# Performance work log

Measured on AMD Instinct MI355X. Metric: run time of the kernel, lower is better.

The kernel has to match this reference:

```python
import jax, jax.numpy as jnp
import numpy as np

B, S, D = 2, 1024, 1024
H, HD = 16, 64          # n_heads, head_dim (H*HD == D)
E, FF = 8, 2816         # num_experts, moe hidden_dim
TOP_K = 2               # hard-coded torch.topk(scores, 2)
EPS = 1e-5


def rmsnorm(x, w):
    return x * jax.lax.rsqrt(jnp.mean(x * x, axis=-1, keepdims=True) + EPS) * w


def apply_rope(x, cos, sin):
    # x: [B,S,H,HD]; cos/sin: [S,HD//2] -> interleaved rotary (llama style)
    xr, xi = x[..., 0::2], x[..., 1::2]
    c = cos[None, :, None, :]
    s = sin[None, :, None, :]
    out_r = xr * c - xi * s
    out_i = xr * s + xi * c
    return jnp.stack([out_r, out_i], axis=-1).reshape(x.shape)


def setup_inputs() -> dict:
    key = jax.random.key(0)
    ks = jax.random.split(key, 10)
    sc = 0.02
    pos = jnp.arange(S, dtype=jnp.float32)
    inv = 1.0 / (10000.0 ** (jnp.arange(0, HD, 2, dtype=jnp.float32) / HD))
    ang = pos[:, None] * inv[None, :]                       # [S, HD//2]
    return {
        "x": jax.random.normal(ks[0], (B, S, D), jnp.float32),
        "freqs_cos": jnp.cos(ang),
        "freqs_sin": jnp.sin(ang),
        "attn_norm_w": jnp.ones((D,), jnp.float32),
        "wq": jax.random.normal(ks[1], (D, D), jnp.float32) * sc,
        "wk": jax.random.normal(ks[2], (D, D), jnp.float32) * sc,
        "wv": jax.random.normal(ks[3], (D, D), jnp.float32) * sc,
        "wo": jax.random.normal(ks[4], (D, D), jnp.float32) * sc,
        "ffn_norm_w": jnp.ones((D,), jnp.float32),
        "gate_w": jax.random.normal(ks[5], (E, D), jnp.float32) * sc,
        "w1": jax.random.normal(ks[6], (E, FF, D), jnp.float32) * sc,
        "w2": jax.random.normal(ks[7], (E, FF, D), jnp.float32) * sc,
        "w3": jax.random.normal(ks[8], (E, FF, D), jnp.float32) * sc,
    }


def reference(x, freqs_cos, freqs_sin, attn_norm_w, wq, wk, wv, wo,
              ffn_norm_w, gate_w, w1, w2, w3):
    b, s, d = x.shape

    # ---- pre-norm attention + residual ----
    xn = rmsnorm(x, attn_norm_w)
    q = (xn @ wq.T).reshape(b, s, H, HD)
    k = (xn @ wk.T).reshape(b, s, H, HD)
    v = (xn @ wv.T).reshape(b, s, H, HD)
    q = apply_rope(q, freqs_cos, freqs_sin)
    k = apply_rope(k, freqs_cos, freqs_sin)
    scores = jnp.einsum("bqhd,bkhd->bhqk", q, k) / jnp.sqrt(jnp.float32(HD))
    causal = jnp.tril(jnp.ones((s, s), bool))
    scores = jnp.where(causal[None, None], scores, jnp.finfo(scores.dtype).min)
    attn = jax.nn.softmax(scores, axis=-1)
    o = jnp.einsum("bhqk,bkhd->bqhd", attn, v).reshape(b, s, d) @ wo.T
    h = x + o

    # ---- top-2 MoE FFN (math identical to gather-per-token einsums) ----
    t = rmsnorm(h, ffn_norm_w).reshape(-1, d)               # [T, D]
    T = t.shape[0]
    gate = t @ gate_w.T                                     # [T, E]
    expert_weights, expert_idx = jax.lax.top_k(gate, TOP_K)
    expert_weights = jax.nn.softmax(expert_weights, axis=-1)  # [T, 2]

    x1 = jax.nn.silu(jnp.einsum("td,efd->tef", t, w1))      # [T, E, FF]
    x3 = jnp.einsum("td,efd->tef", t, w3)                   # [T, E, FF]
    ta = jnp.arange(T)[:, None]
    g = x1[ta, expert_idx] * x3[ta, expert_idx]             # [T, 2, FF]
    gw = g * expert_weights[..., None]                      # fold routing weights
    h_full = jnp.zeros((T, E, FF), t.dtype).at[ta, expert_idx].add(gw)
    moe = jnp.einsum("tef,efd->td", h_full, w2)             # [T, D]

    return h + moe.reshape(b, s, d)
```

## Files before the change

kernel.cpp:

```cpp
#include <hip/hip_runtime.h>

#define DI __device__ __forceinline__

typedef __attribute__((ext_vector_type(8))) short short8;
typedef __attribute__((ext_vector_type(4))) float f32x4;

#define DM   1024
#define TT   2048
#define SEQ  1024
#define NHD  16
#define HDD  64
#define NE   8
#define FF   2816

DI ushort f2bf(float f){
  union { float f; unsigned u; } c; c.f = f;
  unsigned u = c.u;
  u += 0x7fffu + ((u >> 16) & 1u);
  return (ushort)(u >> 16);
}
DI float bf2f(ushort b){
  union { unsigned u; float f; } c; c.u = ((unsigned)b) << 16;
  return c.f;
}
DI unsigned pk2(float a, float b){ return (unsigned)f2bf(a) | ((unsigned)f2bf(b) << 16); }
DI uint2 mku2(unsigned a, unsigned b){ uint2 r; r.x = a; r.y = b; return r; }

DI f32x4 MFMA(short8 a, short8 b, f32x4 c){
  return __builtin_amdgcn_mfma_f32_16x16x32_bf16(a, b, c, 0, 0, 0);
}

DI void gload16(const void* g, void* l){
  __builtin_amdgcn_global_load_lds(
      (const __attribute__((address_space(1))) unsigned*)g,
      (__attribute__((address_space(3))) unsigned*)l, 16, 0, 0);
}

#define LDSWZB(row, p) (((row) * 128) + ((((p) ^ ((row) & 7))) * 16))
#define WZ32(row, p)   (((row) * 256) + ((((p) ^ ((row) & 7))) * 16))

__global__ __launch_bounds__(256) void k_rmsnorm(const float* __restrict__ x,
                                                 const float* __restrict__ w,
                                                 ushort* __restrict__ xh,
                                                 ushort* __restrict__ xl)
{
  int row = blockIdx.x, tid = threadIdx.x;
  float4 v = ((const float4*)(x + (size_t)row * DM))[tid];
  float ss = v.x*v.x + v.y*v.y + v.z*v.z + v.w*v.w;
#pragma unroll
  for (int m = 32; m >= 1; m >>= 1) ss += __shfl_xor(ss, m);
  __shared__ float sh[4];
  if ((tid & 63) == 0) sh[tid >> 6] = ss;
  __syncthreads();
  ss = sh[0] + sh[1] + sh[2] + sh[3];
  float rstd = 1.0f / sqrtf(ss * (1.0f / DM) + 1e-5f);
  float4 wv = ((const float4*)w)[tid];
  float o0 = v.x * rstd * wv.x, o1 = v.y * rstd * wv.y;
  float o2 = v.z * rstd * wv.z, o3 = v.w * rstd * wv.w;
  ushort h0 = f2bf(o0), h1 = f2bf(o1), h2 = f2bf(o2), h3 = f2bf(o3);
  ((uint2*)(xh + (size_t)row * DM))[tid] =
      mku2((unsigned)h0 | ((unsigned)h1 << 16), (unsigned)h2 | ((unsigned)h3 << 16));
  ((uint2*)(xl + (size_t)row * DM))[tid] =
      mku2(pk2(o0 - bf2f(h0), o1 - bf2f(h1)), pk2(o2 - bf2f(h2), o3 - bf2f(h3)));
}

__global__ __launch_bounds__(256) void k_wsplit(
    const float* __restrict__ wq, const float* __restrict__ wk,
    const float* __restrict__ wv, const float* __restrict__ wo,
    ushort* __restrict__ qh, ushort* __restrict__ ql,
    ushort* __restrict__ kh, ushort* __restrict__ kl,
    ushort* __restrict__ vh, ushort* __restrict__ vl,
    ushort* __restrict__ oh, ushort* __restrict__ ol)
{
  int y = blockIdx.y;
  const float* W = y == 0 ? wq : (y == 1 ? wk : (y == 2 ? wv : wo));
  ushort* H = y == 0 ? qh : (y == 1 ? kh : (y == 2 ? vh : oh));
  ushort* L = y == 0 ? ql : (y == 1 ? kl : (y == 2 ? vl : ol));
  int i = blockIdx.x * 256 + threadIdx.x;
  float4 v = ((const float4*)W)[i];
  ushort h0 = f2bf(v.x), h1 = f2bf(v.y), h2 = f2bf(v.z), h3 = f2bf(v.w);
  ((uint2*)H)[i] = mku2((unsigned)h0 | ((unsigned)h1 << 16),
                        (unsigned)h2 | ((unsigned)h3 << 16));
  ((uint2*)L)[i] = mku2(pk2(v.x - bf2f(h0), v.y - bf2f(h1)),
                        pk2(v.z - bf2f(h2), v.w - bf2f(h3)));
}

__global__ __launch_bounds__(256, 2) void k_gemm_qkv(
    const ushort* __restrict__ xh, const ushort* __restrict__ xl,
    const ushort* __restrict__ wqh, const ushort* __restrict__ wql,
    const ushort* __restrict__ wkh, const ushort* __restrict__ wkl,
    const ushort* __restrict__ wvh, const ushort* __restrict__ wvl,
    float* __restrict__ qf, float* __restrict__ kf,
    ushort* __restrict__ vh, ushort* __restrict__ vl)
{
  __shared__ __align__(16) char lds[65536];
  char* Ah = lds;          char* Al = lds + 16384;
  char* Bh = lds + 32768;  char* Bl = lds + 49152;
  int bn = blockIdx.x, bm = blockIdx.y;
  int which = bn >> 3, bnn = bn & 7;
  const ushort* WH = which == 0 ? wqh : (which == 1 ? wkh : wvh);
  const ushort* WL = which == 0 ? wql : (which == 1 ? wkl : wvl);
  int tid = threadIdx.x, lane = tid & 63, w = tid >> 6, wr = w >> 1, wc = w & 1;
  int r0 = lane >> 3, pp = lane & 7;
  size_t asrc[4], bsrc[4]; int cdst[4];
#pragma unroll
  for (int i = 0; i < 4; i++) {
    int c = w * 4 + i;
    int row = c * 8 + r0;
    asrc[i] = (size_t)(bm * 128 + row) * DM + (pp ^ r0) * 8;
    bsrc[i] = (size_t)(bnn * 128 + row) * DM + (pp ^ r0) * 8;
    cdst[i] = c * 1024;
  }
  f32x4 acc[4][4] = {};
  for (int kb = 0; kb < DM; kb += 64) {
    __syncthreads();
#pragma unroll
    for (int i = 0; i < 4; i++) {
      gload16(xh + asrc[i] + kb, Ah + cdst[i]);
      gload16(xl + asrc[i] + kb, Al + cdst[i]);
      gload16(WH + bsrc[i] + kb, Bh + cdst[i]);
      gload16(WL + bsrc[i] + kb, Bl + cdst[i]);
    }
    __syncthreads();
#pragma unroll
    for (int kk = 0; kk < 2; kk++) {
      int j = kk * 4 + (lane >> 4);
      short8 ar[4], al[4];
#pragma unroll
      for (int mi = 0; mi < 4; mi++) {
        int row = wr * 64 + mi * 16 + (lane & 15);
        ar[mi] = *(const short8*)(Ah + LDSWZB(row, j));
        al[mi] = *(const short8*)(Al + LDSWZB(row, j));
      }
#pragma unroll
      for (int ni = 0; ni < 4; ni++) {
        int n = wc * 64 + ni * 16 + (lane & 15);
        short8 b_h = *(const short8*)(Bh + LDSWZB(n, j));
        short8 b_l = *(const short8*)(Bl + LDSWZB(n, j));
#pragma unroll
        for (int mi = 0; mi < 4; mi++) {
          acc[mi][ni] = MFMA(ar[mi], b_h, acc[mi][ni]);
          acc[mi][ni] = MFMA(al[mi], b_h, acc[mi][ni]);
          acc[mi][ni] = MFMA(ar[mi], b_l, acc[mi][ni]);
        }
      }
    }
  }
#pragma unroll
  for (int mi = 0; mi < 4; mi++)
#pragma unroll
    for (int ni = 0; ni < 4; ni++)
#pragma unroll
      for (int r = 0; r < 4; r++) {
        int rg = bm*128 + wr*64 + mi*16 + (lane >> 4)*4 + r;
        int cg = bnn*128 + wc*64 + ni*16 + (lane & 15);
        float v = acc[mi][ni][r];
        if (which == 0)      qf[(size_t)rg * DM + cg] = v;
        else if (which == 1) kf[(size_t)rg * DM + cg] = v;
        else {
          int b = rg >> 10, s = rg & 1023, hh = cg >> 6, hd = cg & 63;
          size_t o = ((size_t)((b*NHD + hh)*HDD + hd)) * SEQ + s;
          ushort hv = f2bf(v);
          vh[o] = hv; vl[o] = f2bf(v - bf2f(hv));
        }
      }
}

__global__ __launch_bounds__(256) void k_rope(
    const float* __restrict__ qf, const float* __restrict__ kf,
    const float* __restrict__ fc, const float* __restrict__ fs,
    ushort* __restrict__ qh, ushort* __restrict__ ql,
    ushort* __restrict__ kh, ushort* __restrict__ kl)
{
  int t = blockIdx.x, tid = threadIdx.x;
  int b = t >> 10, s = t & 1023;
#pragma unroll
  for (int i = 0; i < 2; i++) {
    int p = tid + i*256;
    int hh = p >> 5, pi = p & 31;
    float c = fc[s*32 + pi], sn = fs[s*32 + pi];
    size_t o = ((size_t)(b*NHD + hh) * SEQ + s) * HDD + pi*2;
    {
      float2 v = *(const float2*)(qf + (size_t)t * DM + hh*HDD + pi*2);
      float r0 = v.x*c - v.y*sn, r1 = v.x*sn + v.y*c;
      ushort a0 = f2bf(r0), a1 = f2bf(r1);
      *(unsigned*)(qh + o) = (unsigned)a0 | ((unsigned)a1 << 16);
      *(unsigned*)(ql + o) = pk2(r0 - bf2f(a0), r1 - bf2f(a1));
    }
    {
      float2 v = *(const float2*)(kf + (size_t)t * DM + hh*HDD + pi*2);
      float r0 = v.x*c - v.y*sn, r1 = v.x*sn + v.y*c;
      ushort a0 = f2bf(r0), a1 = f2bf(r1);
      *(unsigned*)(kh + o) = (unsigned)a0 | ((unsigned)a1 << 16);
      *(unsigned*)(kl + o) = pk2(r0 - bf2f(a0), r1 - bf2f(a1));
    }
  }
}

__global__ __launch_bounds__(256) void k_attn(
    const ushort* __restrict__ qh_, const ushort* __restrict__ ql_,
    const ushort* __restrict__ kh_, const ushort* __restrict__ kl_,
    const ushort* __restrict__ vh_, const ushort* __restrict__ vl_,
    ushort* __restrict__ oh_, ushort* __restrict__ ol_)
{
  __shared__ __align__(16) ushort Kh[64*64], Kl[64*64], Vh[64*64], Vl[64*64];
  __shared__ __align__(16) ushort Ph[4*16*64], Pl[4*16*64];
  int qt = blockIdx.x, bh = blockIdx.y;
  int tid = threadIdx.x, lane = tid & 63, w = tid >> 6;
  short8 qfh[2], qfl[2];
  int qrow = qt*64 + w*16 + (lane & 15);
#pragma unroll
  for (int ks = 0; ks < 2; ks++) {
    size_t g = ((size_t)bh * SEQ + qrow) * HDD + ks*32 + (lane >> 4)*8;
    qfh[ks] = *(const short8*)(qh_ + g);
    qfl[ks] = *(const short8*)(ql_ + g);
  }
  f32x4 oacc[4] = {};
  float mrun[4], lrun[4];
#pragma unroll
  for (int r = 0; r < 4; r++) { mrun[r] = -1e30f; lrun[r] = 0.0f; }

  for (int kt = 0; kt <= qt; kt++) {
    __syncthreads();
#pragma unroll
    for (int i = 0; i < 2; i++) {
      int c = tid + i*256, row = c >> 3, sl = c & 7;
      int d = row*64 + ((sl + row) & 7) * 8;
      size_t gk = ((size_t)bh * SEQ + kt*64 + row) * HDD + sl*8;
      *(uint4*)&Kh[d] = *(const uint4*)(kh_ + gk);
      *(uint4*)&Kl[d] = *(const uint4*)(kl_ + gk);
      size_t gv = ((size_t)bh * HDD + row) * SEQ + kt*64 + sl*8;
      *(uint4*)&Vh[d] = *(const uint4*)(vh_ + gv);
      *(uint4*)&Vl[d] = *(const uint4*)(vl_ + gv);
    }
    __syncthreads();
    f32x4 sa[4] = {};
#pragma unroll
    for (int j = 0; j < 4; j++) {
#pragma unroll
      for (int ks = 0; ks < 2; ks++) {
        int kr = j*16 + (lane & 15);
        int d = kr*64 + (((ks*4 + (lane >> 4)) + kr) & 7) * 8;
        short8 b_h = *(const short8*)&Kh[d];
        short8 b_l = *(const short8*)&Kl[d];
        sa[j] = MFMA(qfh[ks], b_h, sa[j]);
        sa[j] = MFMA(qfl[ks], b_h, sa[j]);
        sa[j] = MFMA(qfh[ks], b_l, sa[j]);
      }
    }
    float sv[4][4];
#pragma unroll
    for (int j = 0; j < 4; j++)
#pragma unroll
      for (int r = 0; r < 4; r++) {
        float xx = sa[j][r] * 0.125f;
        if (kt == qt) {
          int kv = j*16 + (lane & 15), qi = w*16 + (lane >> 4)*4 + r;
          if (kv > qi) xx = -1e30f;
        }
        sv[j][r] = xx;
      }
#pragma unroll
    for (int r = 0; r < 4; r++) {
      float mx = fmaxf(fmaxf(sv[0][r], sv[1][r]), fmaxf(sv[2][r], sv[3][r]));
#pragma unroll
      for (int m = 8; m >= 1; m >>= 1) mx = fmaxf(mx, __shfl_xor(mx, m));
      float mn = fmaxf(mrun[r], mx);
      float alp = __expf(mrun[r] - mn);
      mrun[r] = mn;
      float rs = 0.0f;
#pragma unroll
      for (int j = 0; j < 4; j++) { float pv = __expf(sv[j][r] - mn); sv[j][r] = pv; rs += pv; }
#pragma unroll
      for (int m = 8; m >= 1; m >>= 1) rs += __shfl_xor(rs, m);
      lrun[r] = lrun[r] * alp + rs;
#pragma unroll
      for (int hf = 0; hf < 4; hf++) oacc[hf][r] *= alp;
    }
#pragma unroll
    for (int j = 0; j < 4; j++)
#pragma unroll
      for (int r = 0; r < 4; r++) {
        int row = (lane >> 4)*4 + r, col = j*16 + (lane & 15);
        int d = w*1024 + row*64 + (((col >> 3) ^ (row & 7)) * 8) + (col & 7);
        ushort hv = f2bf(sv[j][r]);
        Ph[d] = hv; Pl[d] = f2bf(sv[j][r] - bf2f(hv));
      }
#pragma unroll
    for (int hf = 0; hf < 4; hf++) {
#pragma unroll
      for (int ks = 0; ks < 2; ks++) {
        int prow = lane & 15;
        int pg = ((ks*4 + (lane >> 4)) ^ (prow & 7)) * 8;
        short8 pfh = *(const short8*)&Ph[w*1024 + prow*64 + pg];
        short8 pfl = *(const short8*)&Pl[w*1024 + prow*64 + pg];
        int vrow = hf*16 + (lane & 15);
        int vd = vrow*64 + (((ks*4 + (lane >> 4)) + vrow) & 7) * 8;
        short8 vfh = *(const short8*)&Vh[vd];
        short8 vfl = *(const short8*)&Vl[vd];
        oacc[hf] = MFMA(pfh, vfh, oacc[hf]);
        oacc[hf] = MFMA(pfl, vfh, oacc[hf]);
        oacc[hf] = MFMA(pfh, vfl, oacc[hf]);
      }
    }
  }
  int b = bh >> 4, h = bh & 15;
#pragma unroll
  for (int r = 0; r < 4; r++) {
    float li = 1.0f / lrun[r];
    int srow = qt*64 + w*16 + (lane >> 4)*4 + r;
#pragma unroll
    for (int hf = 0; hf < 4; hf++) {
      float v = oacc[hf][r] * li;
      size_t o = ((size_t)(b*SEQ + srow)) * DM + h*HDD + hf*16 + (lane & 15);
      ushort hv = f2bf(v);
      oh_[o] = hv; ol_[o] = f2bf(v - bf2f(hv));
    }
  }
}

__global__ __launch_bounds__(256, 2) void k_gemm_wo(
    const ushort* __restrict__ oh, const ushort* __restrict__ ol,
    const ushort* __restrict__ woh, const ushort* __restrict__ wol,
    const float* __restrict__ x, float* __restrict__ hb)
{
  __shared__ __align__(16) char lds[49152];
  char* Ah = lds;          char* Al = lds + 8192;
  char* Bh = lds + 16384;  char* Bl = lds + 32768;
  int bnn = blockIdx.x, bm = blockIdx.y;
  int tid = threadIdx.x, lane = tid & 63, w = tid >> 6;
  int r0 = lane >> 3, pp = lane & 7;
  size_t asrc[2]; int adst[2];
#pragma unroll
  for (int i = 0; i < 2; i++) {
    int c = w * 2 + i;
    int row = c * 8 + r0;
    asrc[i] = (size_t)(bm * 64 + row) * DM + (pp ^ r0) * 8;
    adst[i] = c * 1024;
  }
  size_t bsrc[4]; int bdst[4];
#pragma unroll
  for (int i = 0; i < 4; i++) {
    int c = w * 4 + i;
    int row = c * 8 + r0;
    bsrc[i] = (size_t)(bnn * 128 + row) * DM + (pp ^ r0) * 8;
    bdst[i] = c * 1024;
  }
  f32x4 acc[4][2] = {};
  for (int kb = 0; kb < DM; kb += 64) {
    __syncthreads();
#pragma unroll
    for (int i = 0; i < 2; i++) {
      gload16(oh + asrc[i] + kb, Ah + adst[i]);
      gload16(ol + asrc[i] + kb, Al + adst[i]);
    }
#pragma unroll
    for (int i = 0; i < 4; i++) {
      gload16(woh + bsrc[i] + kb, Bh + bdst[i]);
      gload16(wol + bsrc[i] + kb, Bl + bdst[i]);
    }
    __syncthreads();
#pragma unroll
    for (int kk = 0; kk < 2; kk++) {
      int j = kk * 4 + (lane >> 4);
      short8 ar[4], al[4];
#pragma unroll
      for (int mi = 0; mi < 4; mi++) {
        int row = mi * 16 + (lane & 15);
        ar[mi] = *(const short8*)(Ah + LDSWZB(row, j));
        al[mi] = *(const short8*)(Al + LDSWZB(row, j));
      }
#pragma unroll
      for (int ni = 0; ni < 2; ni++) {
        int n = w * 32 + ni * 16 + (lane & 15);
        short8 b_h = *(const short8*)(Bh + LDSWZB(n, j));
        short8 b_l = *(const short8*)(Bl + LDSWZB(n, j));
#pragma unroll
        for (int mi = 0; mi < 4; mi++) {
          acc[mi][ni] = MFMA(ar[mi], b_h, acc[mi][ni]);
          acc[mi][ni] = MFMA(al[mi], b_h, acc[mi][ni]);
          acc[mi][ni] = MFMA(ar[mi], b_l, acc[mi][ni]);
        }
      }
    }
  }
#pragma unroll
  for (int mi = 0; mi < 4; mi++)
#pragma unroll
    for (int ni = 0; ni < 2; ni++)
#pragma unroll
      for (int r = 0; r < 4; r++) {
        int rg = bm*64 + mi*16 + (lane >> 4)*4 + r;
        int cg = bnn*128 + w*32 + ni*16 + (lane & 15);
        hb[(size_t)rg * DM + cg] = x[(size_t)rg * DM + cg] + acc[mi][ni][r];
      }
}

__global__ __launch_bounds__(256) void k_gate(
    const float* __restrict__ hb, const float* __restrict__ fw, const float* __restrict__ gwt,
    ushort* __restrict__ tb, int* __restrict__ idx, float* __restrict__ ew, int* __restrict__ cnt)
{
  int t = blockIdx.x, tid = threadIdx.x;
  float4 v = ((const float4*)(hb + (size_t)t * DM))[tid];
  float ss = v.x*v.x + v.y*v.y + v.z*v.z + v.w*v.w;
#pragma unroll
  for (int m = 32; m >= 1; m >>= 1) ss += __shfl_xor(ss, m);
  __shared__ float sh[4];
  if ((tid & 63) == 0) sh[tid >> 6] = ss;
  __syncthreads();
  ss = sh[0] + sh[1] + sh[2] + sh[3];
  float rstd = 1.0f / sqrtf(ss * (1.0f / DM) + 1e-5f);
  float4 wv = ((const float4*)fw)[tid];
  float tv0 = v.x*rstd*wv.x, tv1 = v.y*rstd*wv.y, tv2 = v.z*rstd*wv.z, tv3 = v.w*rstd*wv.w;
  ((uint2*)(tb + (size_t)t * DM))[tid] = mku2(pk2(tv0, tv1), pk2(tv2, tv3));
  float ge[8];
#pragma unroll
  for (int e = 0; e < 8; e++) {
    float4 gv = ((const float4*)(gwt + (size_t)e * DM))[tid];
    float s = tv0*gv.x + tv1*gv.y + tv2*gv.z + tv3*gv.w;
#pragma unroll
    for (int m = 32; m >= 1; m >>= 1) s += __shfl_xor(s, m);
    ge[e] = s;
  }
  __shared__ float gsh[4][8];
  if ((tid & 63) == 0) {
#pragma unroll
    for (int e = 0; e < 8; e++) gsh[tid >> 6][e] = ge[e];
  }
  __syncthreads();
  if (tid == 0) {
    float lg[8];
#pragma unroll
    for (int e = 0; e < 8; e++) lg[e] = gsh[0][e] + gsh[1][e] + gsh[2][e] + gsh[3][e];
    int i0 = 0;
    for (int e = 1; e < 8; e++) if (lg[e] > lg[i0]) i0 = e;
    int i1 = (i0 == 0) ? 1 : 0;
    for (int e = 0; e < 8; e++) if (e != i0 && lg[e] > lg[i1]) i1 = e;
    float ex = __expf(lg[i1] - lg[i0]);
    idx[2*t] = i0; idx[2*t+1] = i1;
    ew[2*t] = 1.0f / (1.0f + ex); ew[2*t+1] = ex / (1.0f + ex);
    atomicAdd(&cnt[i0], 1); atomicAdd(&cnt[i1], 1);
  }
}

__global__ void k_offsets(const int* __restrict__ cnt, int* __restrict__ off, int* __restrict__ fil)
{
  if (threadIdx.x == 0 && blockIdx.x == 0) {
    int a = 0;
    for (int e = 0; e < 8; e++) { off[e] = a; a += cnt[e]; fil[e] = 0; }
  }
}

__global__ __launch_bounds__(256) void k_scatter(
    const int* __restrict__ idx, const int* __restrict__ off,
    int* __restrict__ fil, int* __restrict__ ent, int* __restrict__ pos)
{
  int t = blockIdx.x * 256 + threadIdx.x;
  if (t < TT) {
#pragma unroll
    for (int k = 0; k < 2; k++) {
      int e = idx[2*t + k];
      int p = atomicAdd(&fil[e], 1);
      int g = off[e] + p;
      ent[g] = 2*t + k;
      pos[2*t + k] = g;
    }
  }
}

__global__ __launch_bounds__(256) void k_tw2(const float* __restrict__ w2, ushort* __restrict__ w2t)
{
  int dt = blockIdx.x, ft = blockIdx.y, e = blockIdx.z;
  __shared__ ushort lt[64*72];
  int tid = threadIdx.x;
#pragma unroll
  for (int i = 0; i < 4; i++) {
    int c = tid + i*256;
    int r = c >> 4, q = c & 15;
    float4 v = *(const float4*)(w2 + ((size_t)e*FF + ft*64 + r) * DM + dt*64 + q*4);
    lt[(q*4+0)*72 + r] = f2bf(v.x);
    lt[(q*4+1)*72 + r] = f2bf(v.y);
    lt[(q*4+2)*72 + r] = f2bf(v.z);
    lt[(q*4+3)*72 + r] = f2bf(v.w);
  }
  __syncthreads();
#pragma unroll
  for (int i = 0; i < 2; i++) {
    int c = tid + i*256;
    int d = c >> 3, fq = c & 7;
    *(uint4*)(w2t + ((size_t)e*DM + dt*64 + d) * FF + ft*64 + fq*8) = *(const uint4*)&lt[d*72 + fq*8];
  }
}

__global__ __launch_bounds__(512, 4) void k_moe13(
    const ushort* __restrict__ tb, const float* __restrict__ w1, const float* __restrict__ w3,
    const int* __restrict__ ent, const float* __restrict__ ew,
    const int* __restrict__ cnt, const int* __restrict__ off,
    ushort* __restrict__ gb)
{
  int nt = blockIdx.x, mt = blockIdx.y, e = blockIdx.z;
  int cn = cnt[e];
  if (mt * 256 >= cn) return;
  int oe = off[e];
  __shared__ __align__(16) char lds[65536];
  char* Ab = lds;
  char* B1 = lds + 32768;
  char* B3 = lds + 49152;
  int tid = threadIdx.x, lane = tid & 63, w = tid >> 6;
  int wr = w >> 1, wc = w & 1;

  int r0 = lane >> 3, pp = lane & 7;
  const ushort* abase = tb + (pp ^ r0) * 8;
  unsigned aoff[4];
#pragma unroll
  for (int i = 0; i < 4; i++) {
    int c = w * 4 + i;
    int r = c * 8 + r0;
    int g = oe + mt * 256 + r; if (g > 2*TT - 1) g = 2*TT - 1;
    aoff[i] = (unsigned)((ent[g] >> 1) * DM);
  }
  int br0 = lane >> 4, bpp = lane & 15;
  size_t bofs[2]; int bdst[2];
#pragma unroll
  for (int i = 0; i < 2; i++) {
    int c = w * 2 + i;
    int row = c * 4 + br0;
    bofs[i] = ((size_t)e * FF + nt * 64 + row) * DM + (bpp ^ (row & 7)) * 4;
    bdst[i] = c * 1024;
  }

  f32x4 acc1[4][2] = {}, acc3[4][2] = {};

  for (int kb = 0; kb < DM; kb += 64) {
    __syncthreads();
#pragma unroll
    for (int i = 0; i < 4; i++)
      gload16(abase + aoff[i] + kb, Ab + (w * 4 + i) * 1024);
#pragma unroll
    for (int i = 0; i < 2; i++) {
      gload16(w1 + bofs[i] + kb, B1 + bdst[i]);
      gload16(w3 + bofs[i] + kb, B3 + bdst[i]);
    }
    __syncthreads();
#pragma unroll
    for (int kk = 0; kk < 2; kk++) {
      int j = kk * 4 + (lane >> 4);
      short8 af[4];
#pragma unroll
      for (int mi = 0; mi < 4; mi++) {
        int row = wr * 64 + mi * 16 + (lane & 15);
        af[mi] = *(const short8*)(Ab + LDSWZB(row, j));
      }
#pragma unroll
      for (int ni = 0; ni < 2; ni++) {
        int n = wc * 32 + ni * 16 + (lane & 15);
        float4 lo1 = *(const float4*)(B1 + WZ32(n, 2*j));
        float4 hi1 = *(const float4*)(B1 + WZ32(n, 2*j + 1));
        float4 lo3 = *(const float4*)(B3 + WZ32(n, 2*j));
        float4 hi3 = *(const float4*)(B3 + WZ32(n, 2*j + 1));
        uint4 u1, u3;
        u1.x = pk2(lo1.x, lo1.y); u1.y = pk2(lo1.z, lo1.w);
        u1.z = pk2(hi1.x, hi1.y); u1.w = pk2(hi1.z, hi1.w);
        u3.x = pk2(lo3.x, lo3.y); u3.y = pk2(lo3.z, lo3.w);
        u3.z = pk2(hi3.x, hi3.y); u3.w = pk2(hi3.z, hi3.w);
        short8 b1f, b3f;
        *(uint4*)&b1f = u1; *(uint4*)&b3f = u3;
#pragma unroll
        for (int mi = 0; mi < 4; mi++) {
          acc1[mi][ni] = MFMA(af[mi], b1f, acc1[mi][ni]);
          acc3[mi][ni] = MFMA(af[mi], b3f, acc3[mi][ni]);
        }
      }
    }
  }
#pragma unroll
  for (int mi = 0; mi < 4; mi++)
#pragma unroll
    for (int ni = 0; ni < 2; ni++)
#pragma unroll
      for (int r = 0; r < 4; r++) {
        int grow = mt * 256 + wr * 64 + mi * 16 + (lane >> 4) * 4 + r;
        if (grow < cn) {
          int g = oe + grow;
          float gwv = ew[ent[g]];
          int f = nt * 64 + wc * 32 + ni * 16 + (lane & 15);
          float x1 = acc1[mi][ni][r], x3 = acc3[mi][ni][r];
          float sg = x1 / (1.0f + __expf(-x1));
          gb[(size_t)g * FF + f] = f2bf(sg * x3 * gwv);
        }
      }
}

__global__ __launch_bounds__(512, 4) void k_moe2(
    const ushort* __restrict__ gb, const ushort* __restrict__ w2t,
    const int* __restrict__ cnt, const int* __restrict__ off,
    float* __restrict__ mr)
{
  int nt = blockIdx.x, mt = blockIdx.y, e = blockIdx.z;
  int cn = cnt[e];
  if (mt * 256 >= cn) return;
  int oe = off[e];
  __shared__ __align__(16) char lds[40960];
  char* Ab = lds; char* Bb = lds + 32768;
  int tid = threadIdx.x, lane = tid & 63, w = tid >> 6;

  const ushort* abase = gb + (((lane & 7) ^ (lane >> 3)) * 8);
  unsigned aoff[4];
#pragma unroll
  for (int i = 0; i < 4; i++) {
    int c = w * 4 + i;
    int r = c * 8 + (lane >> 3);
    int g = oe + mt * 256 + r; if (g > 2*TT - 1) g = 2*TT - 1;
    aoff[i] = (unsigned)(g * FF);
  }
  const ushort* bsrc = w2t + ((size_t)e * DM + nt * 64 + (w * 8 + (lane >> 3))) * FF
                       + (((lane & 7) ^ (lane >> 3)) * 8);
  void* bdst = Bb + w * 1024;

  f32x4 acc[2][4] = {};
  for (int kb = 0; kb < FF; kb += 64) {
    __syncthreads();
#pragma unroll
    for (int i = 0; i < 4; i++)
      gload16(abase + aoff[i] + kb, Ab + (w * 4 + i) * 1024);
    gload16(bsrc + kb, bdst);
    __syncthreads();
#pragma unroll
    for (int kk = 0; kk < 2; kk++) {
      short8 af[2], bf[4];
#pragma unroll
      for (int mi = 0; mi < 2; mi++) {
        int row = w * 32 + mi * 16 + (lane & 15);
        af[mi] = *(const short8*)(Ab + LDSWZB(row, kk * 4 + (lane >> 4)));
      }
#pragma unroll
      for (int ni = 0; ni < 4; ni++) {
        int n = ni * 16 + (lane & 15);
        bf[ni] = *(const short8*)(Bb + LDSWZB(n, kk * 4 + (lane >> 4)));
      }
#pragma unroll
      for (int ni = 0; ni < 4; ni++)
#pragma unroll
        for (int mi = 0; mi < 2; mi++)
          acc[mi][ni] = MFMA(af[mi], bf[ni], acc[mi][ni]);
    }
  }
#pragma unroll
  for (int mi = 0; mi < 2; mi++)
#pragma unroll
    for (int ni = 0; ni < 4; ni++)
#pragma unroll
      for (int r = 0; r < 4; r++) {
        int grow = mt * 256 + w * 32 + mi * 16 + (lane >> 4) * 4 + r;
        if (grow < cn) {
          int cg = nt * 64 + ni * 16 + (lane & 15);
          mr[(size_t)(oe + grow) * DM + cg] = acc[mi][ni][r];
        }
      }
}

__global__ __launch_bounds__(256) void k_final(
    const float* __restrict__ hb, const float* __restrict__ mr,
    const int* __restrict__ pos, float* __restrict__ out)
{
  int t = blockIdx.x, tid = threadIdx.x;
  int g0 = pos[2*t], g1 = pos[2*t+1];
  float4 a  = ((const float4*)(hb + (size_t)t * DM))[tid];
  float4 m0 = ((const float4*)(mr + (size_t)g0 * DM))[tid];
  float4 m1 = ((const float4*)(mr + (size_t)g1 * DM))[tid];
  float4 o;
  o.x = a.x + m0.x + m1.x; o.y = a.y + m0.y + m1.y;
  o.z = a.z + m0.z + m1.z; o.w = a.w + m0.w + m1.w;
  ((float4*)(out + (size_t)t * DM))[tid] = o;
}

extern "C" void kernel_launch(void* const* d_in, const int* in_sizes, int n_in,
                              void* d_out, int out_size, void* d_ws, size_t ws_size,
                              hipStream_t stream)
{
  const float* x   = (const float*)d_in[0];
  const float* fc  = (const float*)d_in[1];
  const float* fs  = (const float*)d_in[2];
  const float* anw = (const float*)d_in[3];
  const float* wq  = (const float*)d_in[4];
  const float* wk  = (const float*)d_in[5];
  const float* wv  = (const float*)d_in[6];
  const float* wo  = (const float*)d_in[7];
  const float* fnw = (const float*)d_in[8];
  const float* gwm = (const float*)d_in[9];
  const float* w1  = (const float*)d_in[10];
  const float* w2  = (const float*)d_in[11];
  const float* w3  = (const float*)d_in[12];
  float* out = (float*)d_out;

  char* p = (char*)d_ws;
  auto alloc = [&](size_t n) { char* r = p; p += (n + 255) & ~(size_t)255; return r; };
  ushort* xnh = (ushort*)alloc((size_t)TT*DM*2);
  ushort* xnl = (ushort*)alloc((size_t)TT*DM*2);
  float*  qf  = (float*) alloc((size_t)TT*DM*4);
  float*  kf  = (float*) alloc((size_t)TT*DM*4);
  ushort* qh  = (ushort*)alloc((size_t)TT*DM*2);
  ushort* ql  = (ushort*)alloc((size_t)TT*DM*2);
  ushort* kh  = (ushort*)alloc((size_t)TT*DM*2);
  ushort* kl  = (ushort*)alloc((size_t)TT*DM*2);
  ushort* vh  = (ushort*)alloc((size_t)TT*DM*2);
  ushort* vl  = (ushort*)alloc((size_t)TT*DM*2);
  ushort* oh  = (ushort*)alloc((size_t)TT*DM*2);
  ushort* ol  = (ushort*)alloc((size_t)TT*DM*2);
  float*  hb  = (float*) alloc((size_t)TT*DM*4);
  ushort* tb  = (ushort*)alloc((size_t)TT*DM*2);
  ushort* w2t = (ushort*)alloc((size_t)NE*FF*DM*2);
  ushort* gb  = (ushort*)alloc((size_t)2*TT*FF*2);
  float*  mr  = (float*) alloc((size_t)2*TT*DM*4);
  int*    idx = (int*)   alloc((size_t)2*TT*4);
  float*  ew  = (float*) alloc((size_t)2*TT*4);
  int*    ent = (int*)   alloc((size_t)2*TT*4);
  int*    pos = (int*)   alloc((size_t)2*TT*4);
  int*    cnt = (int*)   alloc(32);
  int*    off = (int*)   alloc(32);
  int*    fil = (int*)   alloc(32);

  ushort* wsp = (ushort*)mr;
  const size_t WN = (size_t)DM * DM;
  ushort* wqh = wsp;        ushort* wql = wsp + WN;
  ushort* wkh = wsp + 2*WN; ushort* wkl = wsp + 3*WN;
  ushort* wvh = wsp + 4*WN; ushort* wvl = wsp + 5*WN;
  ushort* woh = wsp + 6*WN; ushort* wol = wsp + 7*WN;

  hipMemsetAsync(cnt, 0, 32, stream);
  k_rmsnorm<<<TT, 256, 0, stream>>>(x, anw, xnh, xnl);
  k_wsplit<<<dim3(1024, 4), 256, 0, stream>>>(wq, wk, wv, wo,
      wqh, wql, wkh, wkl, wvh, wvl, woh, wol);
  k_tw2<<<dim3(16, 44, 8), 256, 0, stream>>>(w2, w2t);
  k_gemm_qkv<<<dim3(24, 16), 256, 0, stream>>>(xnh, xnl,
      wqh, wql, wkh, wkl, wvh, wvl, qf, kf, vh, vl);
  k_rope<<<TT, 256, 0, stream>>>(qf, kf, fc, fs, qh, ql, kh, kl);
  k_attn<<<dim3(16, 32), 256, 0, stream>>>(qh, ql, kh, kl, vh, vl, oh, ol);
  k_gemm_wo<<<dim3(8, 32), 256, 0, stream>>>(oh, ol, woh, wol, x, hb);
  k_gate<<<TT, 256, 0, stream>>>(hb, fnw, gwm, tb, idx, ew, cnt);
  k_offsets<<<1, 64, 0, stream>>>(cnt, off, fil);
  k_scatter<<<8, 256, 0, stream>>>(idx, off, fil, ent, pos);
  k_moe13<<<dim3(44, 16, 8), 512, 0, stream>>>(tb, w1, w3, ent, ew, cnt, off, gb);
  k_moe2<<<dim3(16, 16, 8), 512, 0, stream>>>(gb, w2t, cnt, off, mr);
  k_final<<<TT, 256, 0, stream>>>(hb, mr, pos, out);
  (void)in_sizes; (void)n_in; (void)out_size; (void)ws_size;
}
```

Before: 475.7 us.

## Pre-convert MoE w1/w3 to bf16 and load bf16 tiles in expert GEMM

Adds a pass that converts the full w1 and w3 expert weights to bf16 in workspace before the first MoE GEMM. The GEMM then streams bf16 tiles through direct global-to-LDS loads and no longer converts inside its inner loop, which halves B-tile LDS size and traffic. The cost is an extra full read of the fp32 weights plus a bf16 write and re-read on every call. A fallback kernel for small workspaces converts in registers before the LDS store instead. The w1b buffer aliases the start of the workspace, which could collide with other buffers.

```diff
diff --git a/kernel.cpp b/kernel.cpp
--- a/kernel.cpp
+++ b/kernel.cpp
@@ -37,7 +37,6 @@
 }
 
 #define LDSWZB(row, p) (((row) * 128) + ((((p) ^ ((row) & 7))) * 16))
-#define WZ32(row, p)   (((row) * 256) + ((((p) ^ ((row) & 7))) * 16))
 
 __global__ __launch_bounds__(256) void k_rmsnorm(const float* __restrict__ x,
                                                  const float* __restrict__ w,
@@ -85,6 +84,21 @@
                         pk2(v.z - bf2f(h2), v.w - bf2f(h3)));
 }
 
+__global__ __launch_bounds__(256) void k_cw13(const float* __restrict__ w1,
+                                              const float* __restrict__ w3,
+                                              ushort* __restrict__ w1b,
+                                              ushort* __restrict__ w3b)
+{
+  const float* src = blockIdx.y ? w3 : w1;
+  ushort* dst = blockIdx.y ? w3b : w1b;
+  const size_t N4 = (size_t)NE * FF * DM / 4;
+  for (size_t i = (size_t)blockIdx.x * 256 + threadIdx.x; i < N4;
+       i += (size_t)gridDim.x * 256) {
+    float4 v = ((const float4*)src)[i];
+    ((uint2*)dst)[i] = mku2(pk2(v.x, v.y), pk2(v.z, v.w));
+  }
+}
+
 __global__ __launch_bounds__(256, 2) void k_gemm_qkv(
     const ushort* __restrict__ xh, const ushort* __restrict__ xl,
     const ushort* __restrict__ wqh, const ushort* __restrict__ wql,
@@ -493,7 +507,7 @@
 }
 
 __global__ __launch_bounds__(512, 4) void k_moe13(
-    const ushort* __restrict__ tb, const float* __restrict__ w1, const float* __restrict__ w3,
+    const ushort* __restrict__ tb, const ushort* __restrict__ w1b, const ushort* __restrict__ w3b,
     const int* __restrict__ ent, const float* __restrict__ ew,
     const int* __restrict__ cnt, const int* __restrict__ off,
     ushort* __restrict__ gb)
@@ -502,14 +516,14 @@
   int cn = cnt[e];
   if (mt * 256 >= cn) return;
   int oe = off[e];
-  __shared__ __align__(16) char lds[65536];
+  __shared__ __align__(16) char lds[49152];
   char* Ab = lds;
   char* B1 = lds + 32768;
-  char* B3 = lds + 49152;
+  char* B3 = lds + 40960;
   int tid = threadIdx.x, lane = tid & 63, w = tid >> 6;
   int wr = w >> 1, wc = w & 1;
-
   int r0 = lane >> 3, pp = lane & 7;
+
   const ushort* abase = tb + (pp ^ r0) * 8;
   unsigned aoff[4];
 #pragma unroll
@@ -519,15 +533,7 @@
     int g = oe + mt * 256 + r; if (g > 2*TT - 1) g = 2*TT - 1;
     aoff[i] = (unsigned)((ent[g] >> 1) * DM);
   }
-  int br0 = lane >> 4, bpp = lane & 15;
-  size_t bofs[2]; int bdst[2];
-#pragma unroll
-  for (int i = 0; i < 2; i++) {
-    int c = w * 2 + i;
-    int row = c * 4 + br0;
-    bofs[i] = ((size_t)e * FF + nt * 64 + row) * DM + (bpp ^ (row & 7)) * 4;
-    bdst[i] = c * 1024;
-  }
+  size_t bofs = ((size_t)e * FF + nt * 64 + w * 8 + r0) * DM + (pp ^ r0) * 8;
 
   f32x4 acc1[4][2] = {}, acc3[4][2] = {};
 
@@ -536,11 +542,8 @@
 #pragma unroll
     for (int i = 0; i < 4; i++)
       gload16(abase + aoff[i] + kb, Ab + (w * 4 + i) * 1024);
-#pragma unroll
-    for (int i = 0; i < 2; i++) {
-      gload16(w1 + bofs[i] + kb, B1 + bdst[i]);
-      gload16(w3 + bofs[i] + kb, B3 + bdst[i]);
-    }
+    gload16(w1b + bofs + kb, B1 + w * 1024);
+    gload16(w3b + bofs + kb, B3 + w * 1024);
     __syncthreads();
 #pragma unroll
     for (int kk = 0; kk < 2; kk++) {
@@ -554,17 +557,97 @@
 #pragma unroll
       for (int ni = 0; ni < 2; ni++) {
         int n = wc * 32 + ni * 16 + (lane & 15);
-        float4 lo1 = *(const float4*)(B1 + WZ32(n, 2*j));
-        float4 hi1 = *(const float4*)(B1 + WZ32(n, 2*j + 1));
-        float4 lo3 = *(const float4*)(B3 + WZ32(n, 2*j));
-        float4 hi3 = *(const float4*)(B3 + WZ32(n, 2*j + 1));
-        uint4 u1, u3;
-        u1.x = pk2(lo1.x, lo1.y); u1.y = pk2(lo1.z, lo1.w);
-        u1.z = pk2(hi1.x, hi1.y); u1.w = pk2(hi1.z, hi1.w);
-        u3.x = pk2(lo3.x, lo3.y); u3.y = pk2(lo3.z, lo3.w);
-        u3.z = pk2(hi3.x, hi3.y); u3.w = pk2(hi3.z, hi3.w);
-        short8 b1f, b3f;
-        *(uint4*)&b1f = u1; *(uint4*)&b3f = u3;
+        short8 b1f = *(const short8*)(B1 + LDSWZB(n, j));
+        short8 b3f = *(const short8*)(B3 + LDSWZB(n, j));
+#pragma unroll
+        for (int mi = 0; mi < 4; mi++) {
+          acc1[mi][ni] = MFMA(af[mi], b1f, acc1[mi][ni]);
+          acc3[mi][ni] = MFMA(af[mi], b3f, acc3[mi][ni]);
+        }
+      }
+    }
+  }
+#pragma unroll
+  for (int mi = 0; mi < 4; mi++)
+#pragma unroll
+    for (int ni = 0; ni < 2; ni++)
+#pragma unroll
+      for (int r = 0; r < 4; r++) {
+        int grow = mt * 256 + wr * 64 + mi * 16 + (lane >> 4) * 4 + r;
+        if (grow < cn) {
+          int g = oe + grow;
+          float gwv = ew[ent[g]];
+          int f = nt * 64 + wc * 32 + ni * 16 + (lane & 15);
+          float x1 = acc1[mi][ni][r], x3 = acc3[mi][ni][r];
+          float sg = x1 / (1.0f + __expf(-x1));
+          gb[(size_t)g * FF + f] = f2bf(sg * x3 * gwv);
+        }
+      }
+}
+
+__global__ __launch_bounds__(512, 4) void k_moe13f(
+    const ushort* __restrict__ tb, const float* __restrict__ w1, const float* __restrict__ w3,
+    const int* __restrict__ ent, const float* __restrict__ ew,
+    const int* __restrict__ cnt, const int* __restrict__ off,
+    ushort* __restrict__ gb)
+{
+  int nt = blockIdx.x, mt = blockIdx.y, e = blockIdx.z;
+  int cn = cnt[e];
+  if (mt * 256 >= cn) return;
+  int oe = off[e];
+  __shared__ __align__(16) char lds[49152];
+  char* Ab  = lds;
+  char* B1b = lds + 32768;
+  char* B3b = lds + 40960;
+  int tid = threadIdx.x, lane = tid & 63, w = tid >> 6;
+  int wr = w >> 1, wc = w & 1;
+  const ushort* abase = tb + (((lane & 7) ^ (lane >> 3)) * 8);
+  unsigned aoff[4];
+#pragma unroll
+  for (int i = 0; i < 4; i++) {
+    int c = w * 4 + i;
+    int r = c * 8 + (lane >> 3);
+    int g = oe + mt * 256 + r; if (g > 2*TT - 1) g = 2*TT - 1;
+    aoff[i] = (unsigned)((ent[g] >> 1) * DM);
+  }
+  int brow = tid >> 3, bp = tid & 7;
+  const float* b1src = w1 + ((size_t)e * FF + nt * 64 + brow) * DM + bp * 8;
+  const float* b3src = w3 + ((size_t)e * FF + nt * 64 + brow) * DM + bp * 8;
+  int bdst = LDSWZB(brow, bp);
+  f32x4 acc1[4][2] = {}, acc3[4][2] = {};
+  for (int kb = 0; kb < DM; kb += 64) {
+    __syncthreads();
+#pragma unroll
+    for (int i = 0; i < 4; i++)
+      gload16(abase + aoff[i] + kb, Ab + (w * 4 + i) * 1024);
+    {
+      float4 va = *(const float4*)(b1src + kb);
+      float4 vb = *(const float4*)(b1src + kb + 4);
+      float4 vc = *(const float4*)(b3src + kb);
+      float4 vd = *(const float4*)(b3src + kb + 4);
+      uint4 p1, p3;
+      p1.x = pk2(va.x, va.y); p1.y = pk2(va.z, va.w);
+      p1.z = pk2(vb.x, vb.y); p1.w = pk2(vb.z, vb.w);
+      p3.x = pk2(vc.x, vc.y); p3.y = pk2(vc.z, vc.w);
+      p3.z = pk2(vd.x, vd.y); p3.w = pk2(vd.z, vd.w);
+      *(uint4*)(B1b + bdst) = p1;
+      *(uint4*)(B3b + bdst) = p3;
+    }
+    __syncthreads();
+#pragma unroll
+    for (int kk = 0; kk < 2; kk++) {
+      int j = kk * 4 + (lane >> 4);
+      short8 af[4];
+#pragma unroll
+      for (int mi = 0; mi < 4; mi++) {
+        int row = wr * 64 + mi * 16 + (lane & 15);
+        af[mi] = *(const short8*)(Ab + LDSWZB(row, j));
+      }
+#pragma unroll
+      for (int ni = 0; ni < 2; ni++) {
+        int n = wc * 32 + ni * 16 + (lane & 15);
+        short8 b1f = *(const short8*)(B1b + LDSWZB(n, j));
+        short8 b3f = *(const short8*)(B3b + LDSWZB(n, j));
 #pragma unroll
         for (int mi = 0; mi < 4; mi++) {
           acc1[mi][ni] = MFMA(af[mi], b1f, acc1[mi][ni]);
@@ -727,6 +810,10 @@
   ushort* wvh = wsp + 4*WN; ushort* wvl = wsp + 5*WN;
   ushort* woh = wsp + 6*WN; ushort* wol = wsp + 7*WN;
 
+  ushort* w1b = (ushort*)d_ws;
+  ushort* w3b = (ushort*)alloc((size_t)NE*FF*DM*2);
+  bool big_ws = ((size_t)(p - (char*)d_ws) <= ws_size);
+
   hipMemsetAsync(cnt, 0, 32, stream);
   k_rmsnorm<<<TT, 256, 0, stream>>>(x, anw, xnh, xnl);
   k_wsplit<<<dim3(1024, 4), 256, 0, stream>>>(wq, wk, wv, wo,
@@ -740,8 +827,13 @@
   k_gate<<<TT, 256, 0, stream>>>(hb, fnw, gwm, tb, idx, ew, cnt);
   k_offsets<<<1, 64, 0, stream>>>(cnt, off, fil);
   k_scatter<<<8, 256, 0, stream>>>(idx, off, fil, ent, pos);
-  k_moe13<<<dim3(44, 16, 8), 512, 0, stream>>>(tb, w1, w3, ent, ew, cnt, off, gb);
+  if (big_ws) {
+    k_cw13<<<dim3(2048, 2), 256, 0, stream>>>(w1, w3, w1b, w3b);
+    k_moe13<<<dim3(44, 16, 8), 512, 0, stream>>>(tb, w1b, w3b, ent, ew, cnt, off, gb);
+  } else {
+    k_moe13f<<<dim3(44, 16, 8), 512, 0, stream>>>(tb, w1, w3, ent, ew, cnt, off, gb);
+  }
   k_moe2<<<dim3(16, 16, 8), 512, 0, stream>>>(gb, w2t, cnt, off, mr);
   k_final<<<TT, 256, 0, stream>>>(hb, mr, pos, out);
-  (void)in_sizes; (void)n_in; (void)out_size; (void)ws_size;
-}
+  (void)in_sizes; (void)n_in; (void)out_size;
+}
```

Result: no change. 481.9 us (+1.3%).

## Compact MoE tile grid via tile map and convert expert weights to bf16 once per tile

Applied to the files above, without the earlier changes.

Builds a compact list of (expert, row-tile) pairs in k_offsets so the MoE GEMMs launch only as many row blocks as there are active tiles, instead of a dense 16x8 grid where most blocks exit immediately. In k_moe13 the fp32 w1/w3 tiles are now loaded through registers and converted to bf16 once before being stored in LDS. Previously the fp32 tiles were copied into LDS and every wave re-converted them when reading fragments. This halves B-side LDS use and removes redundant conversions, but gives up the async global-to-LDS load path for B. The grid cap of 24 row tiles is assumed to cover every possible routing.

```diff
diff --git a/kernel.cpp b/kernel.cpp
--- a/kernel.cpp
+++ b/kernel.cpp
@@ -37,7 +37,6 @@
 }
 
 #define LDSWZB(row, p) (((row) * 128) + ((((p) ^ ((row) & 7))) * 16))
-#define WZ32(row, p)   (((row) * 256) + ((((p) ^ ((row) & 7))) * 16))
 
 __global__ __launch_bounds__(256) void k_rmsnorm(const float* __restrict__ x,
                                                  const float* __restrict__ w,
@@ -443,11 +442,17 @@
   }
 }
 
-__global__ void k_offsets(const int* __restrict__ cnt, int* __restrict__ off, int* __restrict__ fil)
+__global__ void k_offsets(const int* __restrict__ cnt, int* __restrict__ off,
+                          int* __restrict__ fil, int* __restrict__ tmap)
 {
   if (threadIdx.x == 0 && blockIdx.x == 0) {
-    int a = 0;
-    for (int e = 0; e < 8; e++) { off[e] = a; a += cnt[e]; fil[e] = 0; }
+    int a = 0, nt = 0;
+    for (int e = 0; e < 8; e++) {
+      off[e] = a; a += cnt[e]; fil[e] = 0;
+      int m = (cnt[e] + 255) >> 8;
+      for (int j = 0; j < m; j++) { tmap[1 + nt] = (e << 8) | j; nt++; }
+    }
+    tmap[0] = nt;
   }
 }
 
@@ -495,51 +500,52 @@
 __global__ __launch_bounds__(512, 4) void k_moe13(
     const ushort* __restrict__ tb, const float* __restrict__ w1, const float* __restrict__ w3,
     const int* __restrict__ ent, const float* __restrict__ ew,
-    const int* __restrict__ cnt, const int* __restrict__ off,
+    const int* __restrict__ cnt, const int* __restrict__ off, const int* __restrict__ tmap,
     ushort* __restrict__ gb)
 {
-  int nt = blockIdx.x, mt = blockIdx.y, e = blockIdx.z;
-  int cn = cnt[e];
-  if (mt * 256 >= cn) return;
-  int oe = off[e];
-  __shared__ __align__(16) char lds[65536];
-  char* Ab = lds;
-  char* B1 = lds + 32768;
-  char* B3 = lds + 49152;
+  int y = blockIdx.y;
+  if (y >= tmap[0]) return;
+  int tm = tmap[1 + y];
+  int e = tm >> 8, mt = tm & 255;
+  int nt = blockIdx.x;
+  int cn = cnt[e], oe = off[e];
+  __shared__ __align__(16) char lds[49152];
+  char* Ab  = lds;
+  char* B1b = lds + 32768;
+  char* B3b = lds + 40960;
   int tid = threadIdx.x, lane = tid & 63, w = tid >> 6;
   int wr = w >> 1, wc = w & 1;
-
-  int r0 = lane >> 3, pp = lane & 7;
-  const ushort* abase = tb + (pp ^ r0) * 8;
+  const ushort* abase = tb + (((lane & 7) ^ (lane >> 3)) * 8);
   unsigned aoff[4];
 #pragma unroll
   for (int i = 0; i < 4; i++) {
     int c = w * 4 + i;
-    int r = c * 8 + r0;
+    int r = c * 8 + (lane >> 3);
     int g = oe + mt * 256 + r; if (g > 2*TT - 1) g = 2*TT - 1;
     aoff[i] = (unsigned)((ent[g] >> 1) * DM);
   }
-  int br0 = lane >> 4, bpp = lane & 15;
-  size_t bofs[2]; int bdst[2];
-#pragma unroll
-  for (int i = 0; i < 2; i++) {
-    int c = w * 2 + i;
-    int row = c * 4 + br0;
-    bofs[i] = ((size_t)e * FF + nt * 64 + row) * DM + (bpp ^ (row & 7)) * 4;
-    bdst[i] = c * 1024;
-  }
-
+  int brow = tid >> 3, bp = tid & 7;
+  const float* b1src = w1 + ((size_t)e * FF + nt * 64 + brow) * DM + bp * 8;
+  const float* b3src = w3 + ((size_t)e * FF + nt * 64 + brow) * DM + bp * 8;
+  int bdst = LDSWZB(brow, bp);
   f32x4 acc1[4][2] = {}, acc3[4][2] = {};
-
   for (int kb = 0; kb < DM; kb += 64) {
     __syncthreads();
 #pragma unroll
     for (int i = 0; i < 4; i++)
       gload16(abase + aoff[i] + kb, Ab + (w * 4 + i) * 1024);
-#pragma unroll
-    for (int i = 0; i < 2; i++) {
-      gload16(w1 + bofs[i] + kb, B1 + bdst[i]);
-      gload16(w3 + bofs[i] + kb, B3 + bdst[i]);
+    {
+      float4 va = *(const float4*)(b1src + kb);
+      float4 vb = *(const float4*)(b1src + kb + 4);
+      float4 vc = *(const float4*)(b3src + kb);
+      float4 vd = *(const float4*)(b3src + kb + 4);
+      uint4 p1, p3;
+      p1.x = pk2(va.x, va.y); p1.y = pk2(va.z, va.w);
+      p1.z = pk2(vb.x, vb.y); p1.w = pk2(vb.z, vb.w);
+      p3.x = pk2(vc.x, vc.y); p3.y = pk2(vc.z, vc.w);
+      p3.z = pk2(vd.x, vd.y); p3.w = pk2(vd.z, vd.w);
+      *(uint4*)(B1b + bdst) = p1;
+      *(uint4*)(B3b + bdst) = p3;
     }
     __syncthreads();
 #pragma unroll
@@ -554,17 +560,8 @@
 #pragma unroll
       for (int ni = 0; ni < 2; ni++) {
         int n = wc * 32 + ni * 16 + (lane & 15);
-        float4 lo1 = *(const float4*)(B1 + WZ32(n, 2*j));
-        float4 hi1 = *(const float4*)(B1 + WZ32(n, 2*j + 1));
-        float4 lo3 = *(const float4*)(B3 + WZ32(n, 2*j));
-        float4 hi3 = *(const float4*)(B3 + WZ32(n, 2*j + 1));
-        uint4 u1, u3;
-        u1.x = pk2(lo1.x, lo1.y); u1.y = pk2(lo1.z, lo1.w);
-        u1.z = pk2(hi1.x, hi1.y); u1.w = pk2(hi1.z, hi1.w);
-        u3.x = pk2(lo3.x, lo3.y); u3.y = pk2(lo3.z, lo3.w);
-        u3.z = pk2(hi3.x, hi3.y); u3.w = pk2(hi3.z, hi3.w);
-        short8 b1f, b3f;
-        *(uint4*)&b1f = u1; *(uint4*)&b3f = u3;
+        short8 b1f = *(const short8*)(B1b + LDSWZB(n, j));
+        short8 b3f = *(const short8*)(B3b + LDSWZB(n, j));
 #pragma unroll
         for (int mi = 0; mi < 4; mi++) {
           acc1[mi][ni] = MFMA(af[mi], b1f, acc1[mi][ni]);
@@ -593,13 +590,15 @@
 
 __global__ __launch_bounds__(512, 4) void k_moe2(
     const ushort* __restrict__ gb, const ushort* __restrict__ w2t,
-    const int* __restrict__ cnt, const int* __restrict__ off,
+    const int* __restrict__ cnt, const int* __restrict__ off, const int* __restrict__ tmap,
     float* __restrict__ mr)
 {
-  int nt = blockIdx.x, mt = blockIdx.y, e = blockIdx.z;
-  int cn = cnt[e];
-  if (mt * 256 >= cn) return;
-  int oe = off[e];
+  int y = blockIdx.y;
+  if (y >= tmap[0]) return;
+  int tm = tmap[1 + y];
+  int e = tm >> 8, mt = tm & 255;
+  int nt = blockIdx.x;
+  int cn = cnt[e], oe = off[e];
   __shared__ __align__(16) char lds[40960];
   char* Ab = lds; char* Bb = lds + 32768;
   int tid = threadIdx.x, lane = tid & 63, w = tid >> 6;
@@ -719,6 +718,7 @@
   int*    cnt = (int*)   alloc(32);
   int*    off = (int*)   alloc(32);
   int*    fil = (int*)   alloc(32);
+  int*    tmap= (int*)   alloc(256);
 
   ushort* wsp = (ushort*)mr;
   const size_t WN = (size_t)DM * DM;
@@ -738,10 +738,10 @@
   k_attn<<<dim3(16, 32), 256, 0, stream>>>(qh, ql, kh, kl, vh, vl, oh, ol);
   k_gemm_wo<<<dim3(8, 32), 256, 0, stream>>>(oh, ol, woh, wol, x, hb);
   k_gate<<<TT, 256, 0, stream>>>(hb, fnw, gwm, tb, idx, ew, cnt);
-  k_offsets<<<1, 64, 0, stream>>>(cnt, off, fil);
+  k_offsets<<<1, 64, 0, stream>>>(cnt, off, fil, tmap);
   k_scatter<<<8, 256, 0, stream>>>(idx, off, fil, ent, pos);
-  k_moe13<<<dim3(44, 16, 8), 512, 0, stream>>>(tb, w1, w3, ent, ew, cnt, off, gb);
-  k_moe2<<<dim3(16, 16, 8), 512, 0, stream>>>(gb, w2t, cnt, off, mr);
+  k_moe13<<<dim3(44, 24), 512, 0, stream>>>(tb, w1, w3, ent, ew, cnt, off, tmap, gb);
+  k_moe2<<<dim3(16, 24), 512, 0, stream>>>(gb, w2t, cnt, off, tmap, mr);
   k_final<<<TT, 256, 0, stream>>>(hb, mr, pos, out);
   (void)in_sizes; (void)n_in; (void)out_size; (void)ws_size;
 }
```

Result: faster. 460.1 us (-3.3%).
